# Kernel tuning notes

Hardware: AMD Instinct MI355X
Metric: run time of the kernel (lower is better)

The kernel has to match this reference:

```python
import jax, jax.numpy as jnp
import numpy as np

B, S, DIM = 2, 1024, 1024
E, K, INTER = 16, 2, 512
SHARED_INTER = 2 * INTER  # n_shared_experts * moe_inter_dim
ROUTE_SCALE = 1.0


def setup_inputs() -> dict:
    key = jax.random.key(0)
    ks = jax.random.split(key, 8)
    init = lambda k, shape: jax.random.normal(k, shape, dtype=jnp.float32) * 0.02
    return {
        "x": jax.random.normal(ks[0], (B, S, DIM), dtype=jnp.float32),
        "gate_w": init(ks[1], (E, DIM)),
        "w1": init(ks[2], (E, INTER, DIM)),
        "w2": init(ks[3], (E, DIM, INTER)),
        "w3": init(ks[4], (E, INTER, DIM)),
        "sw1": init(ks[5], (SHARED_INTER, DIM)),
        "sw2": init(ks[6], (DIM, SHARED_INTER)),
        "sw3": init(ks[7], (SHARED_INTER, DIM)),
    }


def reference(x, gate_w, w1, w2, w3, sw1, sw2, sw3):
    b, s, d = x.shape
    xt = x.reshape(-1, d)            # [T, D] flattened tokens
    T = xt.shape[0]

    # Gate: sigmoid scores, top-k experts, normalize selected weights
    scores = jax.nn.sigmoid(xt @ gate_w.T)           # [T, E]
    topv, topi = jax.lax.top_k(scores, K)            # [T, K]
    weights = topv / jnp.sum(topv, axis=-1, keepdims=True) * ROUTE_SCALE

    # Per-token dense combine weights over experts: gate[t, e]
    gate = jnp.zeros((T, E), xt.dtype).at[jnp.arange(T)[:, None], topi].add(weights)

    # Routed experts (SwiGLU), computed densely and combined with gate weights
    h = jax.nn.silu(jnp.einsum('td,eid->tei', xt, w1)) * jnp.einsum('td,eid->tei', xt, w3)
    expert_out = jnp.einsum('tei,edi->ted', h, w2)   # [T, E, D]
    y = jnp.einsum('ted,te->td', expert_out, gate)   # [T, D]

    # Shared expert (SwiGLU MLP over all tokens)
    z = (jax.nn.silu(xt @ sw1.T) * (xt @ sw3.T)) @ sw2.T

    return (y + z).reshape(b, s, d)
```

## Files before the change

### kernel.cpp

```cpp
#include <hip/hip_runtime.h>
#include <stdint.h>

typedef unsigned short u16;
typedef __bf16 bf16x8 __attribute__((ext_vector_type(8)));
typedef float f32x4 __attribute__((ext_vector_type(4)));
typedef unsigned short u16x8 __attribute__((ext_vector_type(8)));

#define TTOK 2048
#define DIMSZ 1024
#define NROUT 16
#define INTERSZ 512

__device__ __forceinline__ u16 f2bf(float f) {
    unsigned int u = __builtin_bit_cast(unsigned int, f);
    unsigned int r = u + 0x7FFFu + ((u >> 16) & 1u);
    return (u16)(r >> 16);
}

__device__ __forceinline__ void gl2lds16(const void* g, void* l) {
    __builtin_amdgcn_global_load_lds(
        (const __attribute__((address_space(1))) void*)(uintptr_t)g,
        (__attribute__((address_space(3))) void*)(uintptr_t)l,
        16, 0, 0);
}

#define NA4 (NROUT * INTERSZ * DIMSZ / 4)
#define NB4 (DIMSZ * DIMSZ / 4)
#define NA8 (NA4 / 2)
#define NR8 ((NA4 + NB4) / 2)
__global__ void cast_all(const float* __restrict__ w1, const float* __restrict__ sw1,
                         const float* __restrict__ w3, const float* __restrict__ sw3,
                         const float* __restrict__ w2, const float* __restrict__ sw2,
                         u16* __restrict__ W1b, u16* __restrict__ W3b,
                         u16* __restrict__ W2b) {
    const int r = blockIdx.y;
    const float* a; const float* b; u16* d;
    if (r == 0)      { a = w1; b = sw1; d = W1b; }
    else if (r == 1) { a = w3; b = sw3; d = W3b; }
    else             { a = w2; b = sw2; d = W2b; }
    for (int j = blockIdx.x * blockDim.x + threadIdx.x; j < NR8;
         j += gridDim.x * blockDim.x) {
        const float4* src = (j < NA8) ? (const float4*)a + 2 * (size_t)j
                                      : (const float4*)b + 2 * (size_t)(j - NA8);
        float4 v0 = src[0], v1 = src[1];
        u16x8 o;
        o[0] = f2bf(v0.x); o[1] = f2bf(v0.y); o[2] = f2bf(v0.z); o[3] = f2bf(v0.w);
        o[4] = f2bf(v1.x); o[5] = f2bf(v1.y); o[6] = f2bf(v1.z); o[7] = f2bf(v1.w);
        *(u16x8*)&d[(size_t)j * 8] = o;
    }
}

__global__ __launch_bounds__(256) void gate_score(
    const float* __restrict__ x, const float* __restrict__ gw,
    int* __restrict__ topi, float2* __restrict__ topw, u16* __restrict__ Xbf) {
    const int t = blockIdx.x;
    const int tid = threadIdx.x;
    const int wave = tid >> 6, lane = tid & 63;
    const int d0 = tid * 4;
    float4 xv = *(const float4*)(x + (size_t)t * DIMSZ + d0);
    ushort4 o;
    o.x = f2bf(xv.x); o.y = f2bf(xv.y); o.z = f2bf(xv.z); o.w = f2bf(xv.w);
    *(ushort4*)&Xbf[(size_t)t * DIMSZ + d0] = o;

    float acc[16];
    #pragma unroll
    for (int e = 0; e < 16; ++e) {
        float4 g = *(const float4*)(gw + e * DIMSZ + d0);
        acc[e] = xv.x * g.x + xv.y * g.y + xv.z * g.z + xv.w * g.w;
    }
    #pragma unroll
    for (int off = 32; off > 0; off >>= 1) {
        #pragma unroll
        for (int e = 0; e < 16; ++e) acc[e] += __shfl_xor(acc[e], off);
    }
    __shared__ float part[4][16];
    __shared__ float sfin[16];
    if (lane < 16) part[wave][lane] = acc[lane];
    __syncthreads();
    if (wave == 0 && lane < 16) {
        float s = part[0][lane] + part[1][lane] + part[2][lane] + part[3][lane];
        sfin[lane] = 1.f / (1.f + expf(-s));
    }
    __syncthreads();
    if (tid == 0) {
        int i0 = 0; float v0 = sfin[0];
        #pragma unroll
        for (int e = 1; e < 16; ++e) { float v = sfin[e]; if (v > v0) { v0 = v; i0 = e; } }
        int i1 = -1; float v1 = -1e30f;
        #pragma unroll
        for (int e = 0; e < 16; ++e) { float v = sfin[e]; if (e != i0 && v > v1) { v1 = v; i1 = e; } }
        float inv = 1.f / (v0 + v1);
        topi[t] = i0 | (i1 << 8);
        topw[t] = make_float2(v0 * inv, v1 * inv);
    }
}

__global__ __launch_bounds__(256) void route_kernel(
    const int* __restrict__ topi, const float2* __restrict__ topw,
    int* __restrict__ counts, int* __restrict__ tokidx, float* __restrict__ tokw) {
    const int e = blockIdx.x;
    const int tid = threadIdx.x;
    int p[8]; int m[8]; int cnt = 0;
    #pragma unroll
    for (int j = 0; j < 8; ++j) {
        int t = tid * 8 + j;
        p[j] = topi[t];
        m[j] = ((p[j] & 255) == e) || ((p[j] >> 8) == e) ? 1 : 0;
        cnt += m[j];
    }
    const int lane = tid & 63, wave = tid >> 6;
    int v = cnt;
    #pragma unroll
    for (int off = 1; off < 64; off <<= 1) {
        int u = __shfl_up(v, off);
        if (lane >= off) v += u;
    }
    __shared__ int wsum[4];
    if (lane == 63) wsum[wave] = v;
    __syncthreads();
    int wbase = 0;
    #pragma unroll
    for (int w = 0; w < 4; ++w) wbase += (w < wave) ? wsum[w] : 0;
    int base = wbase + v - cnt;
    #pragma unroll
    for (int j = 0; j < 8; ++j) {
        if (m[j]) {
            int t = tid * 8 + j;
            float2 w2 = topw[t];
            tokidx[e * TTOK + base] = t;
            tokw[e * TTOK + base] = ((p[j] & 255) == e) ? w2.x : w2.y;
            ++base;
        }
    }
    if (tid == 0) counts[e] = wsum[0] + wsum[1] + wsum[2] + wsum[3];
}

__global__ __launch_bounds__(256) void gemm1s(
    const u16* __restrict__ Xbf, const u16* __restrict__ W1b,
    const u16* __restrict__ W3b, const int* __restrict__ counts,
    const int* __restrict__ tokidx, const float* __restrict__ tokw,
    u16* __restrict__ Hc, u16* __restrict__ Hs) {
    const int e = blockIdx.z;
    const int cnt = (e < NROUT) ? counts[e] : TTOK;
    const int m0 = blockIdx.y * 64;
    if (m0 >= cnt) return;
    const int n0 = blockIdx.x * 128;
    __shared__ u16 As[64 * 64], B1s[128 * 64], B3s[128 * 64];
    const size_t eoff = (size_t)e * INTERSZ * DIMSZ;
    const u16* B1 = W1b + eoff + (size_t)n0 * DIMSZ;
    const u16* B3 = W3b + eoff + (size_t)n0 * DIMSZ;
    const int tid = threadIdx.x;

    int rowa[2], cgsa[2]; size_t arow[2];
    #pragma unroll
    for (int i = 0; i < 2; ++i) {
        int c = tid + i * 256;
        rowa[i] = c >> 3;
        cgsa[i] = ((c & 7) ^ (rowa[i] & 7)) * 8;
        int slot = m0 + rowa[i];
        int g;
        if (e < NROUT) g = (slot < cnt) ? tokidx[e * TTOK + slot] : 0;
        else           g = slot;
        arow[i] = (size_t)g * DIMSZ;
    }
    int rowb[4], cgsb[4];
    #pragma unroll
    for (int i = 0; i < 4; ++i) {
        int c = tid + i * 256;
        rowb[i] = c >> 3;
        cgsb[i] = ((c & 7) ^ (rowb[i] & 7)) * 8;
    }
    f32x4 acc1[2][4] = {}; f32x4 acc3[2][4] = {};
    const int wave = tid >> 6, lane = tid & 63;
    const int wm = (wave >> 1) * 32, wn = (wave & 1) * 64;
    const int lr = lane & 15, lq = lane >> 4;

    for (int kt = 0; kt < DIMSZ / 64; ++kt) {
        const int k0 = kt * 64;
        #pragma unroll
        for (int i = 0; i < 2; ++i) {
            int c = tid + i * 256;
            gl2lds16(Xbf + arow[i] + k0 + cgsa[i], &As[c * 8]);
        }
        #pragma unroll
        for (int i = 0; i < 4; ++i) {
            int c = tid + i * 256;
            int boff = rowb[i] * DIMSZ + k0 + cgsb[i];
            gl2lds16(B1 + boff, &B1s[c * 8]);
            gl2lds16(B3 + boff, &B3s[c * 8]);
        }
        __syncthreads();
        #pragma unroll
        for (int ks = 0; ks < 2; ++ks) {
            bf16x8 af[2], b1f[4], b3f[4];
            const int g = lq + ks * 4;
            #pragma unroll
            for (int mt = 0; mt < 2; ++mt) {
                int m = wm + mt * 16 + lr;
                af[mt] = *(const bf16x8*)&As[(m * 8 + (g ^ (m & 7))) * 8];
            }
            #pragma unroll
            for (int nt = 0; nt < 4; ++nt) {
                int n = wn + nt * 16 + lr;
                int ch = (n * 8 + (g ^ (n & 7))) * 8;
                b1f[nt] = *(const bf16x8*)&B1s[ch];
                b3f[nt] = *(const bf16x8*)&B3s[ch];
            }
            #pragma unroll
            for (int mt = 0; mt < 2; ++mt) {
                #pragma unroll
                for (int nt = 0; nt < 4; ++nt) {
                    acc1[mt][nt] = __builtin_amdgcn_mfma_f32_16x16x32_bf16(af[mt], b1f[nt], acc1[mt][nt], 0, 0, 0);
                    acc3[mt][nt] = __builtin_amdgcn_mfma_f32_16x16x32_bf16(af[mt], b3f[nt], acc3[mt][nt], 0, 0, 0);
                }
            }
        }
        __syncthreads();
    }
    #pragma unroll
    for (int mt = 0; mt < 2; ++mt) {
        #pragma unroll
        for (int nt = 0; nt < 4; ++nt) {
            #pragma unroll
            for (int r = 0; r < 4; ++r) {
                int m = wm + mt * 16 + lq * 4 + r;
                int n = wn + nt * 16 + lr;
                int slot = m0 + m;
                bool valid = slot < cnt;
                float h1 = acc1[mt][nt][r], h3 = acc3[mt][nt][r];
                float hv = 0.f;
                if (valid) {
                    float tw = (e < NROUT) ? tokw[e * TTOK + slot] : 1.0f;
                    hv = h1 / (1.f + __expf(-h1)) * h3 * tw;
                }
                if (e < NROUT)
                    Hc[((size_t)e * TTOK + slot) * INTERSZ + n0 + n] = f2bf(hv);
                else
                    Hs[(size_t)slot * DIMSZ + (e - NROUT) * INTERSZ + n0 + n] = f2bf(hv);
            }
        }
    }
}

__global__ __launch_bounds__(256) void gemm2u(
    const u16* __restrict__ Hc, const u16* __restrict__ Hs,
    const u16* __restrict__ W2b, const u16* __restrict__ W2sb,
    const int* __restrict__ counts, const int* __restrict__ tokidx,
    float* __restrict__ out) {
    const int e = blockIdx.z;
    const bool routed = (e < NROUT);
    const int cnt = routed ? counts[e] : TTOK;
    const int m0 = blockIdx.y * 64;
    if (m0 >= cnt) return;
    const int n0 = blockIdx.x * 64;
    const int klen = routed ? INTERSZ : DIMSZ;
    __shared__ u16 As[64 * 64], Bs[64 * 64];
    const u16* A0 = routed ? Hc + ((size_t)e * TTOK + m0) * INTERSZ
                           : Hs + (size_t)m0 * DIMSZ;
    const u16* B0 = routed ? W2b + ((size_t)e * DIMSZ + n0) * INTERSZ
                           : W2sb + (size_t)n0 * DIMSZ;
    const int tid = threadIdx.x;
    const int wave = tid >> 6, lane = tid & 63;
    const int wm = (wave >> 1) * 32, wn = (wave & 1) * 32;
    const int lr = lane & 15, lq = lane >> 4;

    int rowi[2], cgsi[2];
    #pragma unroll
    for (int i = 0; i < 2; ++i) {
        int c = tid + i * 256;
        rowi[i] = c >> 3;
        cgsi[i] = ((c & 7) ^ (rowi[i] & 7)) * 8;
    }

    f32x4 acc[2][2] = {};
    for (int kt = 0; kt < klen / 64; ++kt) {
        const int k0 = kt * 64;
        #pragma unroll
        for (int i = 0; i < 2; ++i) {
            int c = tid + i * 256;
            gl2lds16(A0 + (size_t)rowi[i] * klen + k0 + cgsi[i], &As[c * 8]);
            gl2lds16(B0 + (size_t)rowi[i] * klen + k0 + cgsi[i], &Bs[c * 8]);
        }
        __syncthreads();
        #pragma unroll
        for (int ks = 0; ks < 2; ++ks) {
            bf16x8 af[2], bfr[2];
            const int g = lq + ks * 4;
            #pragma unroll
            for (int mt = 0; mt < 2; ++mt) {
                int m = wm + mt * 16 + lr;
                af[mt] = *(const bf16x8*)&As[(m * 8 + (g ^ (m & 7))) * 8];
            }
            #pragma unroll
            for (int nt = 0; nt < 2; ++nt) {
                int n = wn + nt * 16 + lr;
                bfr[nt] = *(const bf16x8*)&Bs[(n * 8 + (g ^ (n & 7))) * 8];
            }
            #pragma unroll
            for (int mt = 0; mt < 2; ++mt) {
                #pragma unroll
                for (int nt = 0; nt < 2; ++nt) {
                    acc[mt][nt] = __builtin_amdgcn_mfma_f32_16x16x32_bf16(af[mt], bfr[nt], acc[mt][nt], 0, 0, 0);
                }
            }
        }
        __syncthreads();
    }
    #pragma unroll
    for (int mt = 0; mt < 2; ++mt) {
        #pragma unroll
        for (int r = 0; r < 4; ++r) {
            int m = wm + mt * 16 + lq * 4 + r;
            int slot = m0 + m;
            if (slot < cnt) {
                int t = routed ? tokidx[e * TTOK + slot] : slot;
                #pragma unroll
                for (int nt = 0; nt < 2; ++nt) {
                    int n = wn + nt * 16 + lr;
                    unsafeAtomicAdd(&out[(size_t)t * DIMSZ + n0 + n], acc[mt][nt][r]);
                }
            }
        }
    }
}

extern "C" void kernel_launch(void* const* d_in, const int* in_sizes, int n_in,
                              void* d_out, int out_size, void* d_ws, size_t ws_size,
                              hipStream_t stream) {
    const float* x      = (const float*)d_in[0];
    const float* gate_w = (const float*)d_in[1];
    const float* w1     = (const float*)d_in[2];
    const float* w2     = (const float*)d_in[3];
    const float* w3     = (const float*)d_in[4];
    const float* sw1    = (const float*)d_in[5];
    const float* sw2    = (const float*)d_in[6];
    const float* sw3    = (const float*)d_in[7];
    float* out = (float*)d_out;

    char* ws = (char*)d_ws;
    const size_t SZ_W   = (size_t)(NROUT + 2) * INTERSZ * DIMSZ * 2;
    const size_t SZ_XBF = (size_t)TTOK * DIMSZ * 2;
    u16*   W1b    = (u16*)(ws);
    u16*   W3b    = (u16*)(ws + SZ_W);
    u16*   W2all  = (u16*)(ws + 2 * SZ_W);
    u16*   Xbf    = (u16*)(ws + 3 * SZ_W);
    char*  route  = ws + 3 * SZ_W + SZ_XBF;
    int*   counts = (int*)route;
    int*   topi   = (int*)(route + 256);
    float2* topw  = (float2*)(route + 256 + TTOK * 4);
    int*   tokidx = (int*)(route + 256 + TTOK * 12);
    float* tokw   = (float*)(route + 256 + TTOK * 12 + 16 * TTOK * 4);
    char*  hbuf   = route + 256 + TTOK * 12 + 2 * (size_t)16 * TTOK * 4;
    u16*   Hc     = (u16*)hbuf;
    u16*   Hs     = (u16*)(hbuf + (size_t)NROUT * TTOK * INTERSZ * 2);
    u16*   W2sb   = W2all + (size_t)NROUT * DIMSZ * INTERSZ;

    hipMemsetAsync(out, 0, (size_t)TTOK * DIMSZ * 4, stream);
    cast_all<<<dim3(2048, 3), 256, 0, stream>>>(w1, sw1, w3, sw3, w2, sw2, W1b, W3b, W2all);
    gate_score<<<TTOK, 256, 0, stream>>>(x, gate_w, topi, topw, Xbf);
    route_kernel<<<NROUT, 256, 0, stream>>>(topi, topw, counts, tokidx, tokw);
    gemm1s<<<dim3(INTERSZ / 128, TTOK / 64, NROUT + 2), 256, 0, stream>>>(
        Xbf, W1b, W3b, counts, tokidx, tokw, Hc, Hs);
    gemm2u<<<dim3(DIMSZ / 64, TTOK / 64, NROUT + 1), 256, 0, stream>>>(
        Hc, Hs, W2all, W2sb, counts, tokidx, out);
}
```

Measured before the change: 237.0 us.

## Merge weight cast, gate scoring and output zeroing into one prep kernel; widen gemm2 N tile

Combines the weight cast kernel and the gate-score kernel into a single launch with an extra grid row, and moves the output zeroing from a memset into the gate-score blocks. This removes two launches and one memset pass. Separately, the second GEMM's N tile grows from 64 to 128 columns, so each A tile is reused across more MFMAs and there are half as many blocks. The wider tile raises register and LDS use and lowers the block count, which can reduce occupancy.

```diff
diff --git a/kernel.cpp b/kernel.cpp
--- a/kernel.cpp
+++ b/kernel.cpp
@@ -28,35 +28,37 @@
 #define NB4 (DIMSZ * DIMSZ / 4)
 #define NA8 (NA4 / 2)
 #define NR8 ((NA4 + NB4) / 2)
-__global__ void cast_all(const float* __restrict__ w1, const float* __restrict__ sw1,
-                         const float* __restrict__ w3, const float* __restrict__ sw3,
-                         const float* __restrict__ w2, const float* __restrict__ sw2,
-                         u16* __restrict__ W1b, u16* __restrict__ W3b,
-                         u16* __restrict__ W2b) {
+__global__ __launch_bounds__(256) void prep(
+    const float* __restrict__ w1, const float* __restrict__ sw1,
+    const float* __restrict__ w3, const float* __restrict__ sw3,
+    const float* __restrict__ w2, const float* __restrict__ sw2,
+    u16* __restrict__ W1b, u16* __restrict__ W3b, u16* __restrict__ W2b,
+    const float* __restrict__ x, const float* __restrict__ gw,
+    int* __restrict__ topi, float2* __restrict__ topw,
+    u16* __restrict__ Xbf, float* __restrict__ out) {
     const int r = blockIdx.y;
-    const float* a; const float* b; u16* d;
-    if (r == 0)      { a = w1; b = sw1; d = W1b; }
-    else if (r == 1) { a = w3; b = sw3; d = W3b; }
-    else             { a = w2; b = sw2; d = W2b; }
-    for (int j = blockIdx.x * blockDim.x + threadIdx.x; j < NR8;
-         j += gridDim.x * blockDim.x) {
-        const float4* src = (j < NA8) ? (const float4*)a + 2 * (size_t)j
-                                      : (const float4*)b + 2 * (size_t)(j - NA8);
-        float4 v0 = src[0], v1 = src[1];
-        u16x8 o;
-        o[0] = f2bf(v0.x); o[1] = f2bf(v0.y); o[2] = f2bf(v0.z); o[3] = f2bf(v0.w);
-        o[4] = f2bf(v1.x); o[5] = f2bf(v1.y); o[6] = f2bf(v1.z); o[7] = f2bf(v1.w);
-        *(u16x8*)&d[(size_t)j * 8] = o;
-    }
-}
-
-__global__ __launch_bounds__(256) void gate_score(
-    const float* __restrict__ x, const float* __restrict__ gw,
-    int* __restrict__ topi, float2* __restrict__ topw, u16* __restrict__ Xbf) {
+    const int tid = threadIdx.x;
+    if (r < 3) {
+        const float* a; const float* b; u16* d;
+        if (r == 0)      { a = w1; b = sw1; d = W1b; }
+        else if (r == 1) { a = w3; b = sw3; d = W3b; }
+        else             { a = w2; b = sw2; d = W2b; }
+        const int stride = gridDim.x * blockDim.x;
+        for (int j = blockIdx.x * blockDim.x + tid; j < NR8; j += stride) {
+            const float4* src = (j < NA8) ? (const float4*)a + 2 * (size_t)j
+                                          : (const float4*)b + 2 * (size_t)(j - NA8);
+            float4 v0 = src[0], v1 = src[1];
+            u16x8 o;
+            o[0] = f2bf(v0.x); o[1] = f2bf(v0.y); o[2] = f2bf(v0.z); o[3] = f2bf(v0.w);
+            o[4] = f2bf(v1.x); o[5] = f2bf(v1.y); o[6] = f2bf(v1.z); o[7] = f2bf(v1.w);
+            *(u16x8*)&d[(size_t)j * 8] = o;
+        }
+        return;
+    }
     const int t = blockIdx.x;
-    const int tid = threadIdx.x;
     const int wave = tid >> 6, lane = tid & 63;
     const int d0 = tid * 4;
+    *(float4*)(out + (size_t)t * DIMSZ + d0) = make_float4(0.f, 0.f, 0.f, 0.f);
     float4 xv = *(const float4*)(x + (size_t)t * DIMSZ + d0);
     ushort4 o;
     o.x = f2bf(xv.x); o.y = f2bf(xv.y); o.z = f2bf(xv.z); o.w = f2bf(xv.w);
@@ -252,39 +254,50 @@
     const int cnt = routed ? counts[e] : TTOK;
     const int m0 = blockIdx.y * 64;
     if (m0 >= cnt) return;
-    const int n0 = blockIdx.x * 64;
+    const int n0 = blockIdx.x * 128;
     const int klen = routed ? INTERSZ : DIMSZ;
-    __shared__ u16 As[64 * 64], Bs[64 * 64];
+    __shared__ u16 As[64 * 64], Bs[128 * 64];
     const u16* A0 = routed ? Hc + ((size_t)e * TTOK + m0) * INTERSZ
                            : Hs + (size_t)m0 * DIMSZ;
     const u16* B0 = routed ? W2b + ((size_t)e * DIMSZ + n0) * INTERSZ
                            : W2sb + (size_t)n0 * DIMSZ;
     const int tid = threadIdx.x;
     const int wave = tid >> 6, lane = tid & 63;
-    const int wm = (wave >> 1) * 32, wn = (wave & 1) * 32;
+    const int wm = (wave >> 1) * 32, wn = (wave & 1) * 64;
     const int lr = lane & 15, lq = lane >> 4;
 
-    int rowi[2], cgsi[2];
+    int rowa[2], cgsa[2];
     #pragma unroll
     for (int i = 0; i < 2; ++i) {
         int c = tid + i * 256;
-        rowi[i] = c >> 3;
-        cgsi[i] = ((c & 7) ^ (rowi[i] & 7)) * 8;
-    }
-
-    f32x4 acc[2][2] = {};
+        rowa[i] = c >> 3;
+        cgsa[i] = ((c & 7) ^ (rowa[i] & 7)) * 8;
+    }
+    int rowb[4], cgsb[4];
+    #pragma unroll
+    for (int i = 0; i < 4; ++i) {
+        int c = tid + i * 256;
+        rowb[i] = c >> 3;
+        cgsb[i] = ((c & 7) ^ (rowb[i] & 7)) * 8;
+    }
+
+    f32x4 acc[2][4] = {};
     for (int kt = 0; kt < klen / 64; ++kt) {
         const int k0 = kt * 64;
         #pragma unroll
         for (int i = 0; i < 2; ++i) {
             int c = tid + i * 256;
-            gl2lds16(A0 + (size_t)rowi[i] * klen + k0 + cgsi[i], &As[c * 8]);
-            gl2lds16(B0 + (size_t)rowi[i] * klen + k0 + cgsi[i], &Bs[c * 8]);
+            gl2lds16(A0 + (size_t)rowa[i] * klen + k0 + cgsa[i], &As[c * 8]);
+        }
+        #pragma unroll
+        for (int i = 0; i < 4; ++i) {
+            int c = tid + i * 256;
+            gl2lds16(B0 + (size_t)rowb[i] * klen + k0 + cgsb[i], &Bs[c * 8]);
         }
         __syncthreads();
         #pragma unroll
         for (int ks = 0; ks < 2; ++ks) {
-            bf16x8 af[2], bfr[2];
+            bf16x8 af[2], bfr[4];
             const int g = lq + ks * 4;
             #pragma unroll
             for (int mt = 0; mt < 2; ++mt) {
@@ -292,14 +305,14 @@
                 af[mt] = *(const bf16x8*)&As[(m * 8 + (g ^ (m & 7))) * 8];
             }
             #pragma unroll
-            for (int nt = 0; nt < 2; ++nt) {
+            for (int nt = 0; nt < 4; ++nt) {
                 int n = wn + nt * 16 + lr;
                 bfr[nt] = *(const bf16x8*)&Bs[(n * 8 + (g ^ (n & 7))) * 8];
             }
             #pragma unroll
             for (int mt = 0; mt < 2; ++mt) {
                 #pragma unroll
-                for (int nt = 0; nt < 2; ++nt) {
+                for (int nt = 0; nt < 4; ++nt) {
                     acc[mt][nt] = __builtin_amdgcn_mfma_f32_16x16x32_bf16(af[mt], bfr[nt], acc[mt][nt], 0, 0, 0);
                 }
             }
@@ -315,7 +328,7 @@
             if (slot < cnt) {
                 int t = routed ? tokidx[e * TTOK + slot] : slot;
                 #pragma unroll
-                for (int nt = 0; nt < 2; ++nt) {
+                for (int nt = 0; nt < 4; ++nt) {
                     int n = wn + nt * 16 + lr;
                     unsafeAtomicAdd(&out[(size_t)t * DIMSZ + n0 + n], acc[mt][nt][r]);
                 }
@@ -355,12 +368,12 @@
     u16*   Hs     = (u16*)(hbuf + (size_t)NROUT * TTOK * INTERSZ * 2);
     u16*   W2sb   = W2all + (size_t)NROUT * DIMSZ * INTERSZ;
 
-    hipMemsetAsync(out, 0, (size_t)TTOK * DIMSZ * 4, stream);
-    cast_all<<<dim3(2048, 3), 256, 0, stream>>>(w1, sw1, w3, sw3, w2, sw2, W1b, W3b, W2all);
-    gate_score<<<TTOK, 256, 0, stream>>>(x, gate_w, topi, topw, Xbf);
+    prep<<<dim3(2048, 4), 256, 0, stream>>>(
+        w1, sw1, w3, sw3, w2, sw2, W1b, W3b, W2all,
+        x, gate_w, topi, topw, Xbf, out);
     route_kernel<<<NROUT, 256, 0, stream>>>(topi, topw, counts, tokidx, tokw);
     gemm1s<<<dim3(INTERSZ / 128, TTOK / 64, NROUT + 2), 256, 0, stream>>>(
         Xbf, W1b, W3b, counts, tokidx, tokw, Hc, Hs);
-    gemm2u<<<dim3(DIMSZ / 64, TTOK / 64, NROUT + 1), 256, 0, stream>>>(
+    gemm2u<<<dim3(DIMSZ / 128, TTOK / 64, NROUT + 1), 256, 0, stream>>>(
         Hc, Hs, W2all, W2sb, counts, tokidx, out);
 }
```

Result: faster. 230.8 us (-2.6%).
